# Optimization experiments

Hardware: AMD Instinct MI355X
Metric: run time of the kernel (lower is better)

Reference implementation:

```python
import jax, jax.numpy as jnp
import numpy as np

DIM = 128
HEADS = 8
DIM_HEAD = 16
INNER = DIM * DIM_HEAD  # 2048, per source: inner_dim = dim * dim_head
SCALE = DIM ** (-0.5)   # per source: scale = dim ** -0.5


def setup_inputs() -> dict:
    key = jax.random.key(0)
    k1, k2, k3, k4, k5 = jax.random.split(key, 5)
    tensor = jax.random.normal(k1, (4, 4, 1024, DIM), dtype=jnp.float32)
    latents = jax.random.normal(k2, (4, 4, 64, DIM), dtype=jnp.float32)
    # Linear(dim, inner_dim, bias=False) etc.; stored as [in, out] for x @ W
    Wq = jax.random.normal(k3, (DIM, INNER), dtype=jnp.float32) * (DIM ** -0.5)
    Wkv = jax.random.normal(k4, (DIM, 2 * INNER), dtype=jnp.float32) * (DIM ** -0.5)
    Wo = jax.random.normal(k5, (INNER, DIM), dtype=jnp.float32) * (INNER ** -0.5)
    return {"tensor": tensor, "latents": latents, "Wq": Wq, "Wkv": Wkv, "Wo": Wo}


def _split_heads(x):
    # b t n (h d) -> b h t n d
    b, t, n, hd = x.shape
    d = hd // HEADS
    return x.reshape(b, t, n, HEADS, d).transpose(0, 3, 1, 2, 4)


def reference(tensor, latents, Wq, Wkv, Wo):
    q = latents @ Wq                                  # [b,t,nl,inner]
    kv_input = jnp.concatenate((tensor, latents), axis=-2)  # [b,t,nm+nl,dim]
    kv = kv_input @ Wkv
    k, v = jnp.split(kv, 2, axis=-1)
    q, k, v = map(_split_heads, (q, k, v))            # [b,h,t,n,d]
    q = q * SCALE
    sim = jnp.einsum('bhtid,bhtjd->bhtij', q, k)
    attn = jax.nn.softmax(sim, axis=-1)               # stable softmax (matches max-subtraction)
    out = jnp.einsum('bhtij,bhtjd->bhtid', attn, v)
    # b h t n d -> b t n (h d)
    b, h, t, n, d = out.shape
    out = out.transpose(0, 2, 3, 1, 4).reshape(b, t, n, h * d)
    return out @ Wo
```

## Files before the change

### kernel.cpp

```cpp
#include <hip/hip_runtime.h>

typedef __bf16 bf16x8 __attribute__((ext_vector_type(8)));
typedef __bf16 bf16x4 __attribute__((ext_vector_type(4)));
typedef float  f32x4  __attribute__((ext_vector_type(4)));

#define SCALE2 (0.08838834764831845f * 1.4426950408889634f)

__device__ __forceinline__ f32x4 mfma16(bf16x8 a, bf16x8 b, f32x4 c) {
  return __builtin_amdgcn_mfma_f32_16x16x32_bf16(a, b, c, 0, 0, 0);
}

__device__ __forceinline__ void stage_load(const float* __restrict__ src, int tid,
                                           float4 (&r)[4]) {
  const float4* s4 = (const float4*)(src + (size_t)(tid >> 3) * 128 + ((tid & 7) << 4));
  r[0] = s4[0]; r[1] = s4[1]; r[2] = s4[2]; r[3] = s4[3];
}
__device__ __forceinline__ void stage_write(const float4 (&r)[4], __bf16 (*dst)[136],
                                            int tid) {
  const int row = tid >> 3, colb = (tid & 7) << 4;
  bf16x8 lo, hi;
  lo[0] = (__bf16)r[0].x; lo[1] = (__bf16)r[0].y; lo[2] = (__bf16)r[0].z; lo[3] = (__bf16)r[0].w;
  lo[4] = (__bf16)r[1].x; lo[5] = (__bf16)r[1].y; lo[6] = (__bf16)r[1].z; lo[7] = (__bf16)r[1].w;
  hi[0] = (__bf16)r[2].x; hi[1] = (__bf16)r[2].y; hi[2] = (__bf16)r[2].z; hi[3] = (__bf16)r[2].w;
  hi[4] = (__bf16)r[3].x; hi[5] = (__bf16)r[3].y; hi[6] = (__bf16)r[3].z; hi[7] = (__bf16)r[3].w;
  *(bf16x8*)&dst[row][colb]     = lo;
  *(bf16x8*)&dst[row][colb + 8] = hi;
}

__global__ __launch_bounds__(512, 2) void pa_attn(
    const float* __restrict__ tensor,
    const float* __restrict__ latents,
    const float* __restrict__ Wq,
    const float* __restrict__ Wkv,
    __bf16* __restrict__ Opart,
    float* __restrict__ Mpart,
    float* __restrict__ Lpart)
{
  __shared__ __align__(16) __bf16 Xs[64][136];
  __shared__ __align__(16) __bf16 Ks[64][264];
  __shared__ __align__(16) __bf16 Vts[256][72];
  __shared__ __align__(16) __bf16 Ps[8][16][40];

  const int bid = blockIdx.x;
  const int bt  = bid >> 4;
  const int h   = (bid >> 1) & 7;
  const int js  = bid & 1;

  const int tid  = threadIdx.x;
  const int wave = tid >> 6;
  const int lane = tid & 63;
  const int l15  = lane & 15;
  const int lg   = lane >> 4;
  const int it   = wave >> 1;
  const int jsub = wave & 1;

  const float* latBT = latents + (size_t)bt * (64 * 128);
  const float* tenBT = tensor  + (size_t)bt * (1024 * 128);

  {
    float4 st[4];
    stage_load(latBT, tid, st);
    stage_write(st, Xs, tid);
  }
  __syncthreads();

  #pragma unroll
  for (int n = 0; n < 2; ++n) {
    const int nt = wave * 2 + n;
    const int dcol = h * 256 + nt * 16 + l15;
    f32x4 acc[4] = {};
    #pragma unroll
    for (int kb = 0; kb < 4; ++kb) {
      const int c = kb * 32 + lg * 8;
      bf16x8 bf;
      #pragma unroll
      for (int r = 0; r < 8; ++r) bf[r] = (__bf16)Wq[(size_t)(c + r) * 2048 + dcol];
      #pragma unroll
      for (int mt = 0; mt < 4; ++mt) {
        bf16x8 af = *(const bf16x8*)&Xs[mt * 16 + l15][kb * 32 + lg * 8];
        acc[mt] = mfma16(af, bf, acc[mt]);
      }
    }
    #pragma unroll
    for (int mt = 0; mt < 4; ++mt)
      #pragma unroll
      for (int r = 0; r < 4; ++r)
        Ks[mt * 16 + lg * 4 + r][nt * 16 + l15] = (__bf16)(acc[mt][r] * SCALE2);
  }

  bf16x8 wk[2][4], wv[2][4];
  #pragma unroll
  for (int n = 0; n < 2; ++n) {
    const int dcol = h * 256 + (wave * 2 + n) * 16 + l15;
    #pragma unroll
    for (int kb = 0; kb < 4; ++kb) {
      const int c = kb * 32 + lg * 8;
      bf16x8 k8, v8;
      #pragma unroll
      for (int r = 0; r < 8; ++r) {
        k8[r] = (__bf16)Wkv[(size_t)(c + r) * 4096 + dcol];
        v8[r] = (__bf16)Wkv[(size_t)(c + r) * 4096 + 2048 + dcol];
      }
      wk[n][kb] = k8;
      wv[n][kb] = v8;
    }
  }
  __syncthreads();

  bf16x8 qf[8];
  #pragma unroll
  for (int kb = 0; kb < 8; ++kb)
    qf[kb] = *(const bf16x8*)&Ks[it * 16 + l15][kb * 32 + lg * 8];

  {
    float4 st[4];
    if (js == 0) stage_load(tenBT, tid, st);
    __syncthreads();
    if (js == 0) {
      stage_write(st, Xs, tid);
      __syncthreads();
    }
  }

  float mrow[4] = {-INFINITY, -INFINITY, -INFINITY, -INFINITY};
  float lrow[4] = {0.f, 0.f, 0.f, 0.f};
  f32x4 oacc[16] = {};

  const int NT = js ? 8 : 9;
  for (int t8 = 0; t8 < NT; ++t8) {
    const bool pf = (t8 < NT - 1);
    float4 st[4];
    if (pf) stage_load(tenBT + (size_t)((js ? 9 : 1) + t8) * (64 * 128), tid, st);

    #pragma unroll
    for (int mt = 0; mt < 4; ++mt) {
      f32x4 ka[2] = {}, va[2] = {};
      #pragma unroll
      for (int kb = 0; kb < 4; ++kb) {
        bf16x8 af = *(const bf16x8*)&Xs[mt * 16 + l15][kb * 32 + lg * 8];
        #pragma unroll
        for (int n = 0; n < 2; ++n) {
          ka[n] = mfma16(af, wk[n][kb], ka[n]);
          va[n] = mfma16(af, wv[n][kb], va[n]);
        }
      }
      #pragma unroll
      for (int n = 0; n < 2; ++n) {
        const int d = (wave * 2 + n) * 16 + l15;
        const int j = mt * 16 + lg * 4;
        #pragma unroll
        for (int r = 0; r < 4; ++r) Ks[j + r][d] = (__bf16)ka[n][r];
        bf16x4 vp;
        vp[0] = (__bf16)va[n][0]; vp[1] = (__bf16)va[n][1];
        vp[2] = (__bf16)va[n][2]; vp[3] = (__bf16)va[n][3];
        *(bf16x4*)&Vts[d][j] = vp;
      }
    }
    __syncthreads();

    f32x4 sacc[2] = {};
    #pragma unroll
    for (int kb = 0; kb < 8; ++kb) {
      #pragma unroll
      for (int jt = 0; jt < 2; ++jt) {
        bf16x8 kf = *(const bf16x8*)&Ks[jsub * 32 + jt * 16 + l15][kb * 32 + lg * 8];
        sacc[jt] = mfma16(qf[kb], kf, sacc[jt]);
      }
    }

    float alr[4];
    #pragma unroll
    for (int r = 0; r < 4; ++r) {
      float v = fmaxf(sacc[0][r], sacc[1][r]);
      v = fmaxf(v, __shfl_xor(v, 1));
      v = fmaxf(v, __shfl_xor(v, 2));
      v = fmaxf(v, __shfl_xor(v, 4));
      v = fmaxf(v, __shfl_xor(v, 8));
      const float mn = fmaxf(mrow[r], v);
      const float al = exp2f(mrow[r] - mn);
      const float p0 = exp2f(sacc[0][r] - mn);
      const float p1 = exp2f(sacc[1][r] - mn);
      sacc[0][r] = p0; sacc[1][r] = p1;
      float s = p0 + p1;
      s += __shfl_xor(s, 1);
      s += __shfl_xor(s, 2);
      s += __shfl_xor(s, 4);
      s += __shfl_xor(s, 8);
      lrow[r] = lrow[r] * al + s;
      mrow[r] = mn;
      alr[r] = al;
    }

    #pragma unroll
    for (int jt = 0; jt < 2; ++jt)
      #pragma unroll
      for (int r = 0; r < 4; ++r)
        Ps[wave][lg * 4 + r][jt * 16 + l15] = (__bf16)sacc[jt][r];

    if (pf) stage_write(st, Xs, tid);

    #pragma unroll
    for (int dt = 0; dt < 16; ++dt) {
      oacc[dt][0] *= alr[0]; oacc[dt][1] *= alr[1];
      oacc[dt][2] *= alr[2]; oacc[dt][3] *= alr[3];
    }

    asm volatile("s_waitcnt lgkmcnt(0)" ::: "memory");

    bf16x8 pfr = *(const bf16x8*)&Ps[wave][l15][lg * 8];
    #pragma unroll
    for (int dt = 0; dt < 16; ++dt) {
      bf16x8 vb = *(const bf16x8*)&Vts[dt * 16 + l15][jsub * 32 + lg * 8];
      oacc[dt] = mfma16(pfr, vb, oacc[dt]);
    }
    __syncthreads();
  }

  const int jsplit = js * 2 + jsub;
  const size_t ob = ((((size_t)jsplit * 16 + bt) * 8 + h) * 64) * 256;
  #pragma unroll
  for (int dt = 0; dt < 16; ++dt)
    #pragma unroll
    for (int r = 0; r < 4; ++r)
      Opart[ob + (size_t)(it * 16 + lg * 4 + r) * 256 + dt * 16 + l15] =
          (__bf16)oacc[dt][r];

  const size_t mb = (((size_t)jsplit * 16 + bt) * 8 + h) * 64;
  if (l15 == 0) {
    #pragma unroll
    for (int r = 0; r < 4; ++r) {
      Mpart[mb + it * 16 + lg * 4 + r] = mrow[r];
      Lpart[mb + it * 16 + lg * 4 + r] = lrow[r];
    }
  }
}

__global__ __launch_bounds__(256, 2) void pa_proj(
    const __bf16* __restrict__ Opart, const float* __restrict__ Mpart,
    const float* __restrict__ Lpart, const float* __restrict__ Wo,
    float* __restrict__ part)
{
  __shared__ float alf[4][64];
  __shared__ __align__(16) __bf16 Oh[64][264];
  __shared__ __align__(16) __bf16 Ol[64][264];

  const int bid = blockIdx.x;
  const int bt = bid >> 4, h = (bid >> 1) & 7, ch = bid & 1;
  const int tid = threadIdx.x;

  if (tid < 64) {
    const int i = tid;
    float m[4], L[4];
    #pragma unroll
    for (int s = 0; s < 4; ++s) {
      const size_t b = (((size_t)s * 16 + bt) * 8 + h) * 64 + i;
      m[s] = Mpart[b]; L[s] = Lpart[b];
    }
    const float mm = fmaxf(fmaxf(m[0], m[1]), fmaxf(m[2], m[3]));
    float a[4]; float den = 0.f;
    #pragma unroll
    for (int s = 0; s < 4; ++s) { a[s] = exp2f(m[s] - mm); den += a[s] * L[s]; }
    const float inv = 1.0f / den;
    #pragma unroll
    for (int s = 0; s < 4; ++s) alf[s][i] = a[s] * inv;
  }
  __syncthreads();

  #pragma unroll
  for (int k = 0; k < 8; ++k) {
    const int f = tid + k * 256;
    const int i = f >> 5, d8 = f & 31;
    float v[8] = {0.f, 0.f, 0.f, 0.f, 0.f, 0.f, 0.f, 0.f};
    #pragma unroll
    for (int s = 0; s < 4; ++s) {
      const float a = alf[s][i];
      bf16x8 o8 = *(const bf16x8*)&Opart[(((size_t)s * 16 + bt) * 8 + h) * 16384 +
                                         (size_t)i * 256 + d8 * 8];
      #pragma unroll
      for (int e = 0; e < 8; ++e) v[e] += a * (float)o8[e];
    }
    bf16x8 h8, l8;
    #pragma unroll
    for (int e = 0; e < 8; ++e) {
      h8[e] = (__bf16)v[e];
      l8[e] = (__bf16)(v[e] - (float)h8[e]);
    }
    *(bf16x8*)&Oh[i][d8 * 8] = h8;
    *(bf16x8*)&Ol[i][d8 * 8] = l8;
  }
  __syncthreads();

  const int wave = tid >> 6, lane = tid & 63;
  const int l15 = lane & 15, lg = lane >> 4;
  const int ncol = ch * 64 + wave * 16 + l15;
  f32x4 acc[4] = {};
  #pragma unroll
  for (int kb = 0; kb < 8; ++kb) {
    bf16x8 bh, bl;
    #pragma unroll
    for (int r = 0; r < 8; ++r) {
      const float w = Wo[(size_t)(h * 256 + kb * 32 + lg * 8 + r) * 128 + ncol];
      const __bf16 wh = (__bf16)w;
      bh[r] = wh;
      bl[r] = (__bf16)(w - (float)wh);
    }
    #pragma unroll
    for (int mt = 0; mt < 4; ++mt) {
      bf16x8 ah  = *(const bf16x8*)&Oh[mt * 16 + l15][kb * 32 + lg * 8];
      bf16x8 al8 = *(const bf16x8*)&Ol[mt * 16 + l15][kb * 32 + lg * 8];
      acc[mt] = mfma16(ah,  bh, acc[mt]);
      acc[mt] = mfma16(ah,  bl, acc[mt]);
      acc[mt] = mfma16(al8, bh, acc[mt]);
    }
  }
  const size_t pb = ((size_t)h * 16 + bt) * 8192;
  #pragma unroll
  for (int mt = 0; mt < 4; ++mt)
    #pragma unroll
    for (int r = 0; r < 4; ++r)
      part[pb + (size_t)(mt * 16 + lg * 4 + r) * 128 + ncol] = acc[mt][r];
}

__global__ __launch_bounds__(256) void pa_reduce(const float* __restrict__ part,
                                                 float* __restrict__ out) {
  const int idx = blockIdx.x * 256 + threadIdx.x;
  const f32x4* p4 = (const f32x4*)part;
  f32x4 s = p4[idx];
  #pragma unroll
  for (int h = 1; h < 8; ++h) s += p4[(size_t)h * 32768 + idx];
  ((f32x4*)out)[idx] = s;
}

extern "C" void kernel_launch(void* const* d_in, const int* in_sizes, int n_in,
                              void* d_out, int out_size, void* d_ws, size_t ws_size,
                              hipStream_t stream) {
  const float* tensor  = (const float*)d_in[0];
  const float* latents = (const float*)d_in[1];
  const float* Wq      = (const float*)d_in[2];
  const float* Wkv     = (const float*)d_in[3];
  const float* Wo      = (const float*)d_in[4];
  float* out = (float*)d_out;

  __bf16* Opart = (__bf16*)d_ws;
  float* Mpart = (float*)(Opart + (size_t)4 * 16 * 8 * 64 * 256);
  float* Lpart = Mpart + (size_t)4 * 16 * 8 * 64;
  float* part  = Lpart + (size_t)4 * 16 * 8 * 64;

  pa_attn<<<256, 512, 0, stream>>>(tensor, latents, Wq, Wkv, Opart, Mpart, Lpart);
  pa_proj<<<256, 256, 0, stream>>>(Opart, Mpart, Lpart, Wo, part);
  pa_reduce<<<128, 256, 0, stream>>>(part, out);
}
```

Baseline: 128.1 us.

## Software-pipeline K/V projection with double buffers and split output projection by inner-dim half

The attention kernel now double-buffers the X and K tiles. The next tile's K projection is computed while the current tile's scores are in flight, and its V projection after the PV step, with global loads prefetched two tiles ahead. This is meant to overlap projection MFMAs with softmax and attention work and to cut a barrier per iteration. The output-projection kernel now splits the 256-wide head dimension across the two blocks instead of splitting output columns, so each block reads only half of Opart. That doubles the number of partials the reduce kernel must sum and raises LDS use in the attention kernel.

```diff
diff --git a/kernel.cpp b/kernel.cpp
--- a/kernel.cpp
+++ b/kernel.cpp
@@ -36,8 +36,8 @@
     float* __restrict__ Mpart,
     float* __restrict__ Lpart)
 {
-  __shared__ __align__(16) __bf16 Xs[64][136];
-  __shared__ __align__(16) __bf16 Ks[64][264];
+  __shared__ __align__(16) __bf16 Xs[2][64][136];
+  __shared__ __align__(16) __bf16 Ks[2][64][264];
   __shared__ __align__(16) __bf16 Vts[256][72];
   __shared__ __align__(16) __bf16 Ps[8][16][40];
 
@@ -56,11 +56,17 @@
 
   const float* latBT = latents + (size_t)bt * (64 * 128);
   const float* tenBT = tensor  + (size_t)bt * (1024 * 128);
+  const int NT = js ? 8 : 9;
+
+  auto xsrc = [&](int tau) -> const float* {
+    return js ? (tau == 0 ? latBT : tenBT + (size_t)(8 + tau) * (64 * 128))
+              : (tenBT + (size_t)tau * (64 * 128));
+  };
 
   {
     float4 st[4];
     stage_load(latBT, tid, st);
-    stage_write(st, Xs, tid);
+    stage_write(st, Xs[0], tid);
   }
   __syncthreads();
 
@@ -77,7 +83,7 @@
       for (int r = 0; r < 8; ++r) bf[r] = (__bf16)Wq[(size_t)(c + r) * 2048 + dcol];
       #pragma unroll
       for (int mt = 0; mt < 4; ++mt) {
-        bf16x8 af = *(const bf16x8*)&Xs[mt * 16 + l15][kb * 32 + lg * 8];
+        bf16x8 af = *(const bf16x8*)&Xs[0][mt * 16 + l15][kb * 32 + lg * 8];
         acc[mt] = mfma16(af, bf, acc[mt]);
       }
     }
@@ -85,7 +91,7 @@
     for (int mt = 0; mt < 4; ++mt)
       #pragma unroll
       for (int r = 0; r < 4; ++r)
-        Ks[mt * 16 + lg * 4 + r][nt * 16 + l15] = (__bf16)(acc[mt][r] * SCALE2);
+        Ks[0][mt * 16 + lg * 4 + r][nt * 16 + l15] = (__bf16)(acc[mt][r] * SCALE2);
   }
 
   bf16x8 wk[2][4], wv[2][4];
@@ -110,61 +116,85 @@
   bf16x8 qf[8];
   #pragma unroll
   for (int kb = 0; kb < 8; ++kb)
-    qf[kb] = *(const bf16x8*)&Ks[it * 16 + l15][kb * 32 + lg * 8];
+    qf[kb] = *(const bf16x8*)&Ks[0][it * 16 + l15][kb * 32 + lg * 8];
 
   {
     float4 st[4];
-    if (js == 0) stage_load(tenBT, tid, st);
-    __syncthreads();
     if (js == 0) {
-      stage_write(st, Xs, tid);
-      __syncthreads();
-    }
-  }
+      stage_load(xsrc(0), tid, st);
+      stage_write(st, Xs[0], tid);
+    }
+    stage_load(xsrc(1), tid, st);
+    stage_write(st, Xs[1], tid);
+  }
+  __syncthreads();
+
+  #pragma unroll
+  for (int mt = 0; mt < 4; ++mt) {
+    f32x4 ka[2] = {}, va[2] = {};
+    #pragma unroll
+    for (int kb = 0; kb < 4; ++kb) {
+      bf16x8 af = *(const bf16x8*)&Xs[0][mt * 16 + l15][kb * 32 + lg * 8];
+      #pragma unroll
+      for (int n = 0; n < 2; ++n) {
+        ka[n] = mfma16(af, wk[n][kb], ka[n]);
+        va[n] = mfma16(af, wv[n][kb], va[n]);
+      }
+    }
+    #pragma unroll
+    for (int n = 0; n < 2; ++n) {
+      const int d = (wave * 2 + n) * 16 + l15;
+      const int j = mt * 16 + lg * 4;
+      #pragma unroll
+      for (int r = 0; r < 4; ++r) Ks[0][j + r][d] = (__bf16)ka[n][r];
+      bf16x4 vp;
+      vp[0] = (__bf16)va[n][0]; vp[1] = (__bf16)va[n][1];
+      vp[2] = (__bf16)va[n][2]; vp[3] = (__bf16)va[n][3];
+      *(bf16x4*)&Vts[d][j] = vp;
+    }
+  }
+  __syncthreads();
 
   float mrow[4] = {-INFINITY, -INFINITY, -INFINITY, -INFINITY};
   float lrow[4] = {0.f, 0.f, 0.f, 0.f};
   f32x4 oacc[16] = {};
 
-  const int NT = js ? 8 : 9;
-  for (int t8 = 0; t8 < NT; ++t8) {
-    const bool pf = (t8 < NT - 1);
+  for (int t = 0; t < NT; ++t) {
+    const int cb = t & 1;
+    const int nb = cb ^ 1;
+    const bool haveN  = (t + 1 < NT);
+    const bool haveN2 = (t + 2 < NT);
+
     float4 st[4];
-    if (pf) stage_load(tenBT + (size_t)((js ? 9 : 1) + t8) * (64 * 128), tid, st);
-
-    #pragma unroll
-    for (int mt = 0; mt < 4; ++mt) {
-      f32x4 ka[2] = {}, va[2] = {};
-      #pragma unroll
-      for (int kb = 0; kb < 4; ++kb) {
-        bf16x8 af = *(const bf16x8*)&Xs[mt * 16 + l15][kb * 32 + lg * 8];
+    if (haveN2) stage_load(xsrc(t + 2), tid, st);
+
+    f32x4 sacc[2] = {};
+    #pragma unroll
+    for (int kb = 0; kb < 8; ++kb) {
+      #pragma unroll
+      for (int jt = 0; jt < 2; ++jt) {
+        bf16x8 kf = *(const bf16x8*)&Ks[cb][jsub * 32 + jt * 16 + l15][kb * 32 + lg * 8];
+        sacc[jt] = mfma16(qf[kb], kf, sacc[jt]);
+      }
+    }
+
+    if (haveN) {
+      #pragma unroll
+      for (int mt = 0; mt < 4; ++mt) {
+        f32x4 ka[2] = {};
+        #pragma unroll
+        for (int kb = 0; kb < 4; ++kb) {
+          bf16x8 af = *(const bf16x8*)&Xs[nb][mt * 16 + l15][kb * 32 + lg * 8];
+          ka[0] = mfma16(af, wk[0][kb], ka[0]);
+          ka[1] = mfma16(af, wk[1][kb], ka[1]);
+        }
         #pragma unroll
         for (int n = 0; n < 2; ++n) {
-          ka[n] = mfma16(af, wk[n][kb], ka[n]);
-          va[n] = mfma16(af, wv[n][kb], va[n]);
+          const int d = (wave * 2 + n) * 16 + l15;
+          const int j = mt * 16 + lg * 4;
+          #pragma unroll
+          for (int r = 0; r < 4; ++r) Ks[nb][j + r][d] = (__bf16)ka[n][r];
         }
-      }
-      #pragma unroll
-      for (int n = 0; n < 2; ++n) {
-        const int d = (wave * 2 + n) * 16 + l15;
-        const int j = mt * 16 + lg * 4;
-        #pragma unroll
-        for (int r = 0; r < 4; ++r) Ks[j + r][d] = (__bf16)ka[n][r];
-        bf16x4 vp;
-        vp[0] = (__bf16)va[n][0]; vp[1] = (__bf16)va[n][1];
-        vp[2] = (__bf16)va[n][2]; vp[3] = (__bf16)va[n][3];
-        *(bf16x4*)&Vts[d][j] = vp;
-      }
-    }
-    __syncthreads();
-
-    f32x4 sacc[2] = {};
-    #pragma unroll
-    for (int kb = 0; kb < 8; ++kb) {
-      #pragma unroll
-      for (int jt = 0; jt < 2; ++jt) {
-        bf16x8 kf = *(const bf16x8*)&Ks[jsub * 32 + jt * 16 + l15][kb * 32 + lg * 8];
-        sacc[jt] = mfma16(qf[kb], kf, sacc[jt]);
       }
     }
 
@@ -197,7 +227,7 @@
       for (int r = 0; r < 4; ++r)
         Ps[wave][lg * 4 + r][jt * 16 + l15] = (__bf16)sacc[jt][r];
 
-    if (pf) stage_write(st, Xs, tid);
+    if (haveN2) stage_write(st, Xs[cb], tid);
 
     #pragma unroll
     for (int dt = 0; dt < 16; ++dt) {
@@ -212,6 +242,30 @@
     for (int dt = 0; dt < 16; ++dt) {
       bf16x8 vb = *(const bf16x8*)&Vts[dt * 16 + l15][jsub * 32 + lg * 8];
       oacc[dt] = mfma16(pfr, vb, oacc[dt]);
+    }
+
+    __syncthreads();
+
+    if (haveN) {
+      #pragma unroll
+      for (int mt = 0; mt < 4; ++mt) {
+        f32x4 va[2] = {};
+        #pragma unroll
+        for (int kb = 0; kb < 4; ++kb) {
+          bf16x8 af = *(const bf16x8*)&Xs[nb][mt * 16 + l15][kb * 32 + lg * 8];
+          va[0] = mfma16(af, wv[0][kb], va[0]);
+          va[1] = mfma16(af, wv[1][kb], va[1]);
+        }
+        #pragma unroll
+        for (int n = 0; n < 2; ++n) {
+          const int d = (wave * 2 + n) * 16 + l15;
+          const int j = mt * 16 + lg * 4;
+          bf16x4 vp;
+          vp[0] = (__bf16)va[n][0]; vp[1] = (__bf16)va[n][1];
+          vp[2] = (__bf16)va[n][2]; vp[3] = (__bf16)va[n][3];
+          *(bf16x4*)&Vts[d][j] = vp;
+        }
+      }
     }
     __syncthreads();
   }
@@ -241,8 +295,8 @@
     float* __restrict__ part)
 {
   __shared__ float alf[4][64];
-  __shared__ __align__(16) __bf16 Oh[64][264];
-  __shared__ __align__(16) __bf16 Ol[64][264];
+  __shared__ __align__(16) __bf16 Oh[64][136];
+  __shared__ __align__(16) __bf16 Ol[64][136];
 
   const int bid = blockIdx.x;
   const int bt = bid >> 4, h = (bid >> 1) & 7, ch = bid & 1;
@@ -267,15 +321,15 @@
   __syncthreads();
 
   #pragma unroll
-  for (int k = 0; k < 8; ++k) {
+  for (int k = 0; k < 4; ++k) {
     const int f = tid + k * 256;
-    const int i = f >> 5, d8 = f & 31;
+    const int i = f >> 4, d8 = f & 15;
     float v[8] = {0.f, 0.f, 0.f, 0.f, 0.f, 0.f, 0.f, 0.f};
     #pragma unroll
     for (int s = 0; s < 4; ++s) {
       const float a = alf[s][i];
       bf16x8 o8 = *(const bf16x8*)&Opart[(((size_t)s * 16 + bt) * 8 + h) * 16384 +
-                                         (size_t)i * 256 + d8 * 8];
+                                         (size_t)i * 256 + ch * 128 + d8 * 8];
       #pragma unroll
       for (int e = 0; e < 8; ++e) v[e] += a * (float)o8[e];
     }
@@ -292,33 +346,43 @@
 
   const int wave = tid >> 6, lane = tid & 63;
   const int l15 = lane & 15, lg = lane >> 4;
-  const int ncol = ch * 64 + wave * 16 + l15;
-  f32x4 acc[4] = {};
-  #pragma unroll
-  for (int kb = 0; kb < 8; ++kb) {
-    bf16x8 bh, bl;
-    #pragma unroll
-    for (int r = 0; r < 8; ++r) {
-      const float w = Wo[(size_t)(h * 256 + kb * 32 + lg * 8 + r) * 128 + ncol];
-      const __bf16 wh = (__bf16)w;
-      bh[r] = wh;
-      bl[r] = (__bf16)(w - (float)wh);
+  f32x4 acc[4][2] = {};
+  #pragma unroll
+  for (int kb = 0; kb < 4; ++kb) {
+    bf16x8 bh[2], bl[2];
+    #pragma unroll
+    for (int n = 0; n < 2; ++n) {
+      const int ncol = wave * 32 + n * 16 + l15;
+      #pragma unroll
+      for (int r = 0; r < 8; ++r) {
+        const float w =
+            Wo[(size_t)(h * 256 + ch * 128 + kb * 32 + lg * 8 + r) * 128 + ncol];
+        const __bf16 wh = (__bf16)w;
+        bh[n][r] = wh;
+        bl[n][r] = (__bf16)(w - (float)wh);
+      }
     }
     #pragma unroll
     for (int mt = 0; mt < 4; ++mt) {
       bf16x8 ah  = *(const bf16x8*)&Oh[mt * 16 + l15][kb * 32 + lg * 8];
       bf16x8 al8 = *(const bf16x8*)&Ol[mt * 16 + l15][kb * 32 + lg * 8];
-      acc[mt] = mfma16(ah,  bh, acc[mt]);
-      acc[mt] = mfma16(ah,  bl, acc[mt]);
-      acc[mt] = mfma16(al8, bh, acc[mt]);
-    }
-  }
-  const size_t pb = ((size_t)h * 16 + bt) * 8192;
+      #pragma unroll
+      for (int n = 0; n < 2; ++n) {
+        acc[mt][n] = mfma16(ah,  bh[n], acc[mt][n]);
+        acc[mt][n] = mfma16(ah,  bl[n], acc[mt][n]);
+        acc[mt][n] = mfma16(al8, bh[n], acc[mt][n]);
+      }
+    }
+  }
+  const size_t pb = ((size_t)(h * 2 + ch) * 16 + bt) * 8192;
   #pragma unroll
   for (int mt = 0; mt < 4; ++mt)
     #pragma unroll
-    for (int r = 0; r < 4; ++r)
-      part[pb + (size_t)(mt * 16 + lg * 4 + r) * 128 + ncol] = acc[mt][r];
+    for (int n = 0; n < 2; ++n)
+      #pragma unroll
+      for (int r = 0; r < 4; ++r)
+        part[pb + (size_t)(mt * 16 + lg * 4 + r) * 128 + wave * 32 + n * 16 + l15] =
+            acc[mt][n][r];
 }
 
 __global__ __launch_bounds__(256) void pa_reduce(const float* __restrict__ part,
@@ -327,7 +391,7 @@
   const f32x4* p4 = (const f32x4*)part;
   f32x4 s = p4[idx];
   #pragma unroll
-  for (int h = 1; h < 8; ++h) s += p4[(size_t)h * 32768 + idx];
+  for (int g = 1; g < 16; ++g) s += p4[(size_t)g * 32768 + idx];
   ((f32x4*)out)[idx] = s;
 }
 
```

Result: no change. 128.7 us (+0.5%).

## Fold K and V projections into per-head 128x128 weight products and fuse projection

Applied to the files above, without the earlier changes.

A new pre-kernel computes per-head products Wq_h·Wk_hᵀ (scaled) and Wv_h·Wo_h as 128x128 matrices stored as bf16 hi/lo pairs. The attention kernel can then score latents against the raw input tokens directly and accumulate the attention-weighted raw inputs, instead of projecting K and V to 256-dim per head for every tile. It uses MFMA against an identity to transpose input tiles, double-buffers those tiles, merges the two j-halves in shared memory and applies the output projection in place. This removes the separate partial-output kernel and its global round trip. In exchange the weight products are recomputed on every call, the grid drops to 128 blocks, each block walks all 17 tiles serially, and the split-bf16 error-compensating MFMAs add extra work.

```diff
diff --git a/kernel.cpp b/kernel.cpp
--- a/kernel.cpp
+++ b/kernel.cpp
@@ -8,6 +8,56 @@
 
 __device__ __forceinline__ f32x4 mfma16(bf16x8 a, bf16x8 b, f32x4 c) {
   return __builtin_amdgcn_mfma_f32_16x16x32_bf16(a, b, c, 0, 0, 0);
+}
+
+__global__ __launch_bounds__(256, 4) void pa_pre(
+    const float* __restrict__ Wq, const float* __restrict__ Wkv,
+    const float* __restrict__ Wo, __bf16* __restrict__ Mt,
+    __bf16* __restrict__ Nt) {
+  const int g = blockIdx.x;
+  const int mn = g >> 7, h = (g >> 4) & 7, rch = g & 15;
+  const int R = rch * 8;
+  const int tid = threadIdx.x;
+  const int hc = h * 256;
+  __shared__ float Bv[8][260];
+
+  if (mn == 0) {
+    for (int i = tid; i < 8 * 64; i += 256) {
+      const int b = i >> 6, c4 = (i & 63) * 4;
+      const float4 v = *(const float4*)&Wkv[(size_t)(R + b) * 4096 + hc + c4];
+      Bv[b][c4] = v.x; Bv[b][c4 + 1] = v.y; Bv[b][c4 + 2] = v.z; Bv[b][c4 + 3] = v.w;
+    }
+  } else {
+    for (int i = tid; i < 512; i += 256) {
+      const int c = i >> 1, q = (i & 1) * 4;
+      const float4 v = *(const float4*)&Wo[(size_t)(hc + c) * 128 + R + q];
+      Bv[q][c] = v.x; Bv[q + 1][c] = v.y; Bv[q + 2][c] = v.z; Bv[q + 3][c] = v.w;
+    }
+  }
+  __syncthreads();
+
+  const int a  = tid & 127;
+  const int bh = (tid >> 7) * 4;
+  const float* arow = (mn == 0) ? &Wq[(size_t)a * 2048 + hc]
+                                : &Wkv[(size_t)a * 4096 + 2048 + hc];
+  float acc[4] = {0.f, 0.f, 0.f, 0.f};
+  for (int c4 = 0; c4 < 256; c4 += 4) {
+    const float4 av = *(const float4*)&arow[c4];
+    #pragma unroll
+    for (int j = 0; j < 4; ++j)
+      acc[j] += av.x * Bv[bh + j][c4] + av.y * Bv[bh + j][c4 + 1] +
+                av.z * Bv[bh + j][c4 + 2] + av.w * Bv[bh + j][c4 + 3];
+  }
+  __bf16* dsth = (mn == 0 ? Mt : Nt) + (size_t)h * 16384;
+  __bf16* dstl = dsth + (size_t)8 * 16384;
+  const float sc = (mn == 0) ? SCALE2 : 1.0f;
+  #pragma unroll
+  for (int j = 0; j < 4; ++j) {
+    const float v = acc[j] * sc;
+    const __bf16 hi = (__bf16)v;
+    dsth[(size_t)(R + bh + j) * 128 + a] = hi;
+    dstl[(size_t)(R + bh + j) * 128 + a] = (__bf16)(v - (float)hi);
+  }
 }
 
 __device__ __forceinline__ void stage_load(const float* __restrict__ src, int tid,
@@ -15,7 +65,7 @@
   const float4* s4 = (const float4*)(src + (size_t)(tid >> 3) * 128 + ((tid & 7) << 4));
   r[0] = s4[0]; r[1] = s4[1]; r[2] = s4[2]; r[3] = s4[3];
 }
-__device__ __forceinline__ void stage_write(const float4 (&r)[4], __bf16 (*dst)[136],
+__device__ __forceinline__ void stage_write(const float4 (&r)[4], __bf16 (*dst)[152],
                                             int tid) {
   const int row = tid >> 3, colb = (tid & 7) << 4;
   bf16x8 lo, hi;
@@ -27,24 +77,22 @@
   *(bf16x8*)&dst[row][colb + 8] = hi;
 }
 
-__global__ __launch_bounds__(512, 2) void pa_attn(
+__global__ __launch_bounds__(512, 1) void pa_fused(
     const float* __restrict__ tensor,
     const float* __restrict__ latents,
-    const float* __restrict__ Wq,
-    const float* __restrict__ Wkv,
-    __bf16* __restrict__ Opart,
-    float* __restrict__ Mpart,
-    float* __restrict__ Lpart)
+    const __bf16* __restrict__ Mt,
+    const __bf16* __restrict__ Nt,
+    float* __restrict__ part)
 {
-  __shared__ __align__(16) __bf16 Xs[64][136];
-  __shared__ __align__(16) __bf16 Ks[64][264];
-  __shared__ __align__(16) __bf16 Vts[256][72];
+  __shared__ __align__(16) __bf16 Xs[2][64][152];
+  __shared__ __align__(16) __bf16 AsBs[2][64][136];
+  __shared__ __align__(16) __bf16 Xts[2][128][76];
   __shared__ __align__(16) __bf16 Ps[8][16][40];
-
-  const int bid = blockIdx.x;
-  const int bt  = bid >> 4;
-  const int h   = (bid >> 1) & 7;
-  const int js  = bid & 1;
+  __shared__ float Ms[8][16];
+  __shared__ float Ls[8][16];
+
+  const int bt = blockIdx.x & 15;
+  const int h  = blockIdx.x >> 4;
 
   const int tid  = threadIdx.x;
   const int wave = tid >> 6;
@@ -57,116 +105,87 @@
   const float* latBT = latents + (size_t)bt * (64 * 128);
   const float* tenBT = tensor  + (size_t)bt * (1024 * 128);
 
+  bf16x8 ident;
+  #pragma unroll
+  for (int r = 0; r < 8; ++r)
+    ident[r] = (lg * 8 + r == l15) ? (__bf16)1.0f : (__bf16)0.0f;
+
+  for (int i = tid; i < 2 * 64 * 24; i += 512) {
+    const int b = i / 1536, rem = i - b * 1536;
+    Xs[b][rem / 24][128 + rem % 24] = (__bf16)0.0f;
+  }
   {
     float4 st[4];
     stage_load(latBT, tid, st);
-    stage_write(st, Xs, tid);
-  }
-  __syncthreads();
-
-  #pragma unroll
-  for (int n = 0; n < 2; ++n) {
-    const int nt = wave * 2 + n;
-    const int dcol = h * 256 + nt * 16 + l15;
-    f32x4 acc[4] = {};
+    stage_write(st, Xs[0], tid);
+  }
+  __syncthreads();
+
+  {
+    bf16x8 mh[4], ml[4];
+    const __bf16* MtH = Mt + (size_t)h * 16384;
+    const __bf16* MtL = MtH + (size_t)8 * 16384;
     #pragma unroll
     for (int kb = 0; kb < 4; ++kb) {
-      const int c = kb * 32 + lg * 8;
-      bf16x8 bf;
-      #pragma unroll
-      for (int r = 0; r < 8; ++r) bf[r] = (__bf16)Wq[(size_t)(c + r) * 2048 + dcol];
+      mh[kb] = *(const bf16x8*)&MtH[(size_t)(wave * 16 + l15) * 128 + kb * 32 + lg * 8];
+      ml[kb] = *(const bf16x8*)&MtL[(size_t)(wave * 16 + l15) * 128 + kb * 32 + lg * 8];
+    }
+    f32x4 accA[4] = {};
+    #pragma unroll
+    for (int kb = 0; kb < 4; ++kb)
       #pragma unroll
       for (int mt = 0; mt < 4; ++mt) {
-        bf16x8 af = *(const bf16x8*)&Xs[mt * 16 + l15][kb * 32 + lg * 8];
-        acc[mt] = mfma16(af, bf, acc[mt]);
-      }
-    }
+        bf16x8 af = *(const bf16x8*)&Xs[0][mt * 16 + l15][kb * 32 + lg * 8];
+        accA[mt] = mfma16(af, mh[kb], accA[mt]);
+        accA[mt] = mfma16(af, ml[kb], accA[mt]);
+      }
     #pragma unroll
     for (int mt = 0; mt < 4; ++mt)
       #pragma unroll
-      for (int r = 0; r < 4; ++r)
-        Ks[mt * 16 + lg * 4 + r][nt * 16 + l15] = (__bf16)(acc[mt][r] * SCALE2);
-  }
-
-  bf16x8 wk[2][4], wv[2][4];
-  #pragma unroll
-  for (int n = 0; n < 2; ++n) {
-    const int dcol = h * 256 + (wave * 2 + n) * 16 + l15;
-    #pragma unroll
-    for (int kb = 0; kb < 4; ++kb) {
-      const int c = kb * 32 + lg * 8;
-      bf16x8 k8, v8;
-      #pragma unroll
-      for (int r = 0; r < 8; ++r) {
-        k8[r] = (__bf16)Wkv[(size_t)(c + r) * 4096 + dcol];
-        v8[r] = (__bf16)Wkv[(size_t)(c + r) * 4096 + 2048 + dcol];
-      }
-      wk[n][kb] = k8;
-      wv[n][kb] = v8;
-    }
-  }
-  __syncthreads();
-
-  bf16x8 qf[8];
-  #pragma unroll
-  for (int kb = 0; kb < 8; ++kb)
-    qf[kb] = *(const bf16x8*)&Ks[it * 16 + l15][kb * 32 + lg * 8];
-
-  {
-    float4 st[4];
-    if (js == 0) stage_load(tenBT, tid, st);
-    __syncthreads();
-    if (js == 0) {
-      stage_write(st, Xs, tid);
-      __syncthreads();
-    }
+      for (int r = 0; r < 4; ++r) {
+        const float v = accA[mt][r];
+        const __bf16 hi = (__bf16)v;
+        AsBs[0][mt * 16 + lg * 4 + r][wave * 16 + l15] = hi;
+        AsBs[1][mt * 16 + lg * 4 + r][wave * 16 + l15] = (__bf16)(v - (float)hi);
+      }
+  }
+  __syncthreads();
+
+  bf16x8 qh[4], ql[4];
+  #pragma unroll
+  for (int kb = 0; kb < 4; ++kb) {
+    qh[kb] = *(const bf16x8*)&AsBs[0][it * 16 + l15][kb * 32 + lg * 8];
+    ql[kb] = *(const bf16x8*)&AsBs[1][it * 16 + l15][kb * 32 + lg * 8];
   }
 
   float mrow[4] = {-INFINITY, -INFINITY, -INFINITY, -INFINITY};
   float lrow[4] = {0.f, 0.f, 0.f, 0.f};
-  f32x4 oacc[16] = {};
-
-  const int NT = js ? 8 : 9;
-  for (int t8 = 0; t8 < NT; ++t8) {
-    const bool pf = (t8 < NT - 1);
+  f32x4 oacc[8] = {};
+
+  for (int t = 0; t < 17; ++t) {
+    const int cb = t & 1, nb = cb ^ 1;
+    const bool pf = (t < 16);
     float4 st[4];
-    if (pf) stage_load(tenBT + (size_t)((js ? 9 : 1) + t8) * (64 * 128), tid, st);
-
-    #pragma unroll
-    for (int mt = 0; mt < 4; ++mt) {
-      f32x4 ka[2] = {}, va[2] = {};
-      #pragma unroll
-      for (int kb = 0; kb < 4; ++kb) {
-        bf16x8 af = *(const bf16x8*)&Xs[mt * 16 + l15][kb * 32 + lg * 8];
-        #pragma unroll
-        for (int n = 0; n < 2; ++n) {
-          ka[n] = mfma16(af, wk[n][kb], ka[n]);
-          va[n] = mfma16(af, wv[n][kb], va[n]);
-        }
-      }
-      #pragma unroll
-      for (int n = 0; n < 2; ++n) {
-        const int d = (wave * 2 + n) * 16 + l15;
-        const int j = mt * 16 + lg * 4;
-        #pragma unroll
-        for (int r = 0; r < 4; ++r) Ks[j + r][d] = (__bf16)ka[n][r];
-        bf16x4 vp;
-        vp[0] = (__bf16)va[n][0]; vp[1] = (__bf16)va[n][1];
-        vp[2] = (__bf16)va[n][2]; vp[3] = (__bf16)va[n][3];
-        *(bf16x4*)&Vts[d][j] = vp;
-      }
-    }
-    __syncthreads();
+    if (pf) stage_load(tenBT + (size_t)t * (64 * 128), tid, st);
+
+    if (t > 0) {
+      bf16x8 pfr = *(const bf16x8*)&Ps[wave][l15][lg * 8];
+      #pragma unroll
+      for (int dt = 0; dt < 8; ++dt) {
+        bf16x8 vb = *(const bf16x8*)&Xts[nb][dt * 16 + l15][jsub * 32 + lg * 8];
+        oacc[dt] = mfma16(pfr, vb, oacc[dt]);
+      }
+    }
 
     f32x4 sacc[2] = {};
     #pragma unroll
-    for (int kb = 0; kb < 8; ++kb) {
+    for (int kb = 0; kb < 4; ++kb)
       #pragma unroll
       for (int jt = 0; jt < 2; ++jt) {
-        bf16x8 kf = *(const bf16x8*)&Ks[jsub * 32 + jt * 16 + l15][kb * 32 + lg * 8];
-        sacc[jt] = mfma16(qf[kb], kf, sacc[jt]);
-      }
-    }
+        bf16x8 kf = *(const bf16x8*)&Xs[cb][jsub * 32 + jt * 16 + l15][kb * 32 + lg * 8];
+        sacc[jt] = mfma16(qh[kb], kf, sacc[jt]);
+        sacc[jt] = mfma16(ql[kb], kf, sacc[jt]);
+      }
 
     float alr[4];
     #pragma unroll
@@ -176,10 +195,10 @@
       v = fmaxf(v, __shfl_xor(v, 2));
       v = fmaxf(v, __shfl_xor(v, 4));
       v = fmaxf(v, __shfl_xor(v, 8));
-      const float mn = fmaxf(mrow[r], v);
-      const float al = exp2f(mrow[r] - mn);
-      const float p0 = exp2f(sacc[0][r] - mn);
-      const float p1 = exp2f(sacc[1][r] - mn);
+      const float mn2 = fmaxf(mrow[r], v);
+      const float al = exp2f(mrow[r] - mn2);
+      const float p0 = exp2f(sacc[0][r] - mn2);
+      const float p1 = exp2f(sacc[1][r] - mn2);
       sacc[0][r] = p0; sacc[1][r] = p1;
       float s = p0 + p1;
       s += __shfl_xor(s, 1);
@@ -187,7 +206,7 @@
       s += __shfl_xor(s, 4);
       s += __shfl_xor(s, 8);
       lrow[r] = lrow[r] * al + s;
-      mrow[r] = mn;
+      mrow[r] = mn2;
       alr[r] = al;
     }
 
@@ -197,128 +216,122 @@
       for (int r = 0; r < 4; ++r)
         Ps[wave][lg * 4 + r][jt * 16 + l15] = (__bf16)sacc[jt][r];
 
-    if (pf) stage_write(st, Xs, tid);
-
-    #pragma unroll
-    for (int dt = 0; dt < 16; ++dt) {
+    #pragma unroll
+    for (int dt = 0; dt < 8; ++dt) {
       oacc[dt][0] *= alr[0]; oacc[dt][1] *= alr[1];
       oacc[dt][2] *= alr[2]; oacc[dt][3] *= alr[3];
     }
 
-    asm volatile("s_waitcnt lgkmcnt(0)" ::: "memory");
-
+    #pragma unroll
+    for (int ds = 0; ds < 4; ++ds) {
+      const int dbase = ((wave & 1) * 4 + ds) * 16;
+      bf16x8 at = *(const bf16x8*)&Xs[cb][(wave >> 1) * 16 + l15][dbase + lg * 8];
+      f32x4 tp = mfma16(at, ident, (f32x4){0.f, 0.f, 0.f, 0.f});
+      bf16x4 tb;
+      tb[0] = (__bf16)tp[0]; tb[1] = (__bf16)tp[1];
+      tb[2] = (__bf16)tp[2]; tb[3] = (__bf16)tp[3];
+      *(bf16x4*)&Xts[cb][dbase + l15][(wave >> 1) * 16 + lg * 4] = tb;
+    }
+
+    if (pf) stage_write(st, Xs[nb], tid);
+    __syncthreads();
+  }
+
+  {
     bf16x8 pfr = *(const bf16x8*)&Ps[wave][l15][lg * 8];
     #pragma unroll
-    for (int dt = 0; dt < 16; ++dt) {
-      bf16x8 vb = *(const bf16x8*)&Vts[dt * 16 + l15][jsub * 32 + lg * 8];
+    for (int dt = 0; dt < 8; ++dt) {
+      bf16x8 vb = *(const bf16x8*)&Xts[0][dt * 16 + l15][jsub * 32 + lg * 8];
       oacc[dt] = mfma16(pfr, vb, oacc[dt]);
     }
-    __syncthreads();
-  }
-
-  const int jsplit = js * 2 + jsub;
-  const size_t ob = ((((size_t)jsplit * 16 + bt) * 8 + h) * 64) * 256;
-  #pragma unroll
-  for (int dt = 0; dt < 16; ++dt)
-    #pragma unroll
-    for (int r = 0; r < 4; ++r)
-      Opart[ob + (size_t)(it * 16 + lg * 4 + r) * 256 + dt * 16 + l15] =
-          (__bf16)oacc[dt][r];
-
-  const size_t mb = (((size_t)jsplit * 16 + bt) * 8 + h) * 64;
-  if (l15 == 0) {
+  }
+
+  if (l15 == 0)
     #pragma unroll
     for (int r = 0; r < 4; ++r) {
-      Mpart[mb + it * 16 + lg * 4 + r] = mrow[r];
-      Lpart[mb + it * 16 + lg * 4 + r] = lrow[r];
-    }
-  }
-}
-
-__global__ __launch_bounds__(256, 2) void pa_proj(
-    const __bf16* __restrict__ Opart, const float* __restrict__ Mpart,
-    const float* __restrict__ Lpart, const float* __restrict__ Wo,
-    float* __restrict__ part)
-{
-  __shared__ float alf[4][64];
-  __shared__ __align__(16) __bf16 Oh[64][264];
-  __shared__ __align__(16) __bf16 Ol[64][264];
-
-  const int bid = blockIdx.x;
-  const int bt = bid >> 4, h = (bid >> 1) & 7, ch = bid & 1;
-  const int tid = threadIdx.x;
-
-  if (tid < 64) {
-    const int i = tid;
-    float m[4], L[4];
-    #pragma unroll
-    for (int s = 0; s < 4; ++s) {
-      const size_t b = (((size_t)s * 16 + bt) * 8 + h) * 64 + i;
-      m[s] = Mpart[b]; L[s] = Lpart[b];
-    }
-    const float mm = fmaxf(fmaxf(m[0], m[1]), fmaxf(m[2], m[3]));
-    float a[4]; float den = 0.f;
-    #pragma unroll
-    for (int s = 0; s < 4; ++s) { a[s] = exp2f(m[s] - mm); den += a[s] * L[s]; }
-    const float inv = 1.0f / den;
-    #pragma unroll
-    for (int s = 0; s < 4; ++s) alf[s][i] = a[s] * inv;
-  }
-  __syncthreads();
-
-  #pragma unroll
-  for (int k = 0; k < 8; ++k) {
-    const int f = tid + k * 256;
-    const int i = f >> 5, d8 = f & 31;
-    float v[8] = {0.f, 0.f, 0.f, 0.f, 0.f, 0.f, 0.f, 0.f};
-    #pragma unroll
-    for (int s = 0; s < 4; ++s) {
-      const float a = alf[s][i];
-      bf16x8 o8 = *(const bf16x8*)&Opart[(((size_t)s * 16 + bt) * 8 + h) * 16384 +
-                                         (size_t)i * 256 + d8 * 8];
-      #pragma unroll
-      for (int e = 0; e < 8; ++e) v[e] += a * (float)o8[e];
-    }
-    bf16x8 h8, l8;
-    #pragma unroll
-    for (int e = 0; e < 8; ++e) {
-      h8[e] = (__bf16)v[e];
-      l8[e] = (__bf16)(v[e] - (float)h8[e]);
-    }
-    *(bf16x8*)&Oh[i][d8 * 8] = h8;
-    *(bf16x8*)&Ol[i][d8 * 8] = l8;
-  }
-  __syncthreads();
-
-  const int wave = tid >> 6, lane = tid & 63;
-  const int l15 = lane & 15, lg = lane >> 4;
-  const int ncol = ch * 64 + wave * 16 + l15;
-  f32x4 acc[4] = {};
-  #pragma unroll
-  for (int kb = 0; kb < 8; ++kb) {
-    bf16x8 bh, bl;
-    #pragma unroll
-    for (int r = 0; r < 8; ++r) {
-      const float w = Wo[(size_t)(h * 256 + kb * 32 + lg * 8 + r) * 128 + ncol];
-      const __bf16 wh = (__bf16)w;
-      bh[r] = wh;
-      bl[r] = (__bf16)(w - (float)wh);
-    }
-    #pragma unroll
-    for (int mt = 0; mt < 4; ++mt) {
-      bf16x8 ah  = *(const bf16x8*)&Oh[mt * 16 + l15][kb * 32 + lg * 8];
-      bf16x8 al8 = *(const bf16x8*)&Ol[mt * 16 + l15][kb * 32 + lg * 8];
-      acc[mt] = mfma16(ah,  bh, acc[mt]);
-      acc[mt] = mfma16(ah,  bl, acc[mt]);
-      acc[mt] = mfma16(al8, bh, acc[mt]);
-    }
-  }
-  const size_t pb = ((size_t)h * 16 + bt) * 8192;
-  #pragma unroll
-  for (int mt = 0; mt < 4; ++mt)
-    #pragma unroll
-    for (int r = 0; r < 4; ++r)
-      part[pb + (size_t)(mt * 16 + lg * 4 + r) * 128 + ncol] = acc[mt][r];
+      Ms[wave][lg * 4 + r] = mrow[r];
+      Ls[wave][lg * 4 + r] = lrow[r];
+    }
+  __syncthreads();
+
+  float alm[4], linv[4];
+  #pragma unroll
+  for (int r = 0; r < 4; ++r) {
+    const float mo = Ms[wave ^ 1][lg * 4 + r];
+    const float ms = fmaxf(mrow[r], mo);
+    alm[r] = exp2f(mrow[r] - ms);
+    const float alo = exp2f(mo - ms);
+    linv[r] = 1.0f / (alm[r] * lrow[r] + alo * Ls[wave ^ 1][lg * 4 + r]);
+  }
+  #pragma unroll
+  for (int dt = 0; dt < 8; ++dt) {
+    oacc[dt][0] *= alm[0]; oacc[dt][1] *= alm[1];
+    oacc[dt][2] *= alm[2]; oacc[dt][3] *= alm[3];
+  }
+  float* Os = (float*)&AsBs[0][0][0];
+  {
+    const int oh = (jsub ^ 1) * 4;
+    #pragma unroll
+    for (int dtl = 0; dtl < 4; ++dtl)
+      #pragma unroll
+      for (int r = 0; r < 4; ++r)
+        Os[(size_t)(it * 16 + lg * 4 + r) * 132 + (oh + dtl) * 16 + l15] =
+            oacc[oh + dtl][r];
+  }
+  __syncthreads();
+  float merged[4][4];
+  {
+    const int oh = jsub * 4;
+    #pragma unroll
+    for (int dtl = 0; dtl < 4; ++dtl)
+      #pragma unroll
+      for (int r = 0; r < 4; ++r)
+        merged[dtl][r] =
+            (oacc[oh + dtl][r] +
+             Os[(size_t)(it * 16 + lg * 4 + r) * 132 + (oh + dtl) * 16 + l15]) *
+            linv[r];
+  }
+  __syncthreads();
+  #pragma unroll
+  for (int dtl = 0; dtl < 4; ++dtl)
+    #pragma unroll
+    for (int r = 0; r < 4; ++r) {
+      const float v = merged[dtl][r];
+      const __bf16 hi = (__bf16)v;
+      AsBs[0][it * 16 + lg * 4 + r][jsub * 64 + dtl * 16 + l15] = hi;
+      AsBs[1][it * 16 + lg * 4 + r][jsub * 64 + dtl * 16 + l15] =
+          (__bf16)(v - (float)hi);
+    }
+  __syncthreads();
+
+  {
+    bf16x8 nh[4], nl[4];
+    const __bf16* NtH = Nt + (size_t)h * 16384;
+    const __bf16* NtL = NtH + (size_t)8 * 16384;
+    #pragma unroll
+    for (int kb = 0; kb < 4; ++kb) {
+      nh[kb] = *(const bf16x8*)&NtH[(size_t)(wave * 16 + l15) * 128 + kb * 32 + lg * 8];
+      nl[kb] = *(const bf16x8*)&NtL[(size_t)(wave * 16 + l15) * 128 + kb * 32 + lg * 8];
+    }
+    f32x4 pacc[4] = {};
+    #pragma unroll
+    for (int kb = 0; kb < 4; ++kb)
+      #pragma unroll
+      for (int mt = 0; mt < 4; ++mt) {
+        bf16x8 ah = *(const bf16x8*)&AsBs[0][mt * 16 + l15][kb * 32 + lg * 8];
+        bf16x8 al = *(const bf16x8*)&AsBs[1][mt * 16 + l15][kb * 32 + lg * 8];
+        pacc[mt] = mfma16(ah, nh[kb], pacc[mt]);
+        pacc[mt] = mfma16(al, nh[kb], pacc[mt]);
+        pacc[mt] = mfma16(ah, nl[kb], pacc[mt]);
+      }
+    const size_t pb = ((size_t)h * 16 + bt) * 8192;
+    #pragma unroll
+    for (int mt = 0; mt < 4; ++mt)
+      #pragma unroll
+      for (int r = 0; r < 4; ++r)
+        part[pb + (size_t)(mt * 16 + lg * 4 + r) * 128 + wave * 16 + l15] =
+            pacc[mt][r];
+  }
 }
 
 __global__ __launch_bounds__(256) void pa_reduce(const float* __restrict__ part,
@@ -327,7 +340,7 @@
   const f32x4* p4 = (const f32x4*)part;
   f32x4 s = p4[idx];
   #pragma unroll
-  for (int h = 1; h < 8; ++h) s += p4[(size_t)h * 32768 + idx];
+  for (int g = 1; g < 8; ++g) s += p4[(size_t)g * 32768 + idx];
   ((f32x4*)out)[idx] = s;
 }
 
@@ -341,12 +354,11 @@
   const float* Wo      = (const float*)d_in[4];
   float* out = (float*)d_out;
 
-  __bf16* Opart = (__bf16*)d_ws;
-  float* Mpart = (float*)(Opart + (size_t)4 * 16 * 8 * 64 * 256);
-  float* Lpart = Mpart + (size_t)4 * 16 * 8 * 64;
-  float* part  = Lpart + (size_t)4 * 16 * 8 * 64;
-
-  pa_attn<<<256, 512, 0, stream>>>(tensor, latents, Wq, Wkv, Opart, Mpart, Lpart);
-  pa_proj<<<256, 256, 0, stream>>>(Opart, Mpart, Lpart, Wo, part);
+  __bf16* Mt  = (__bf16*)d_ws;
+  __bf16* Nt  = Mt + (size_t)2 * 8 * 128 * 128;
+  float*  part = (float*)(Nt + (size_t)2 * 8 * 128 * 128);
+
+  pa_pre<<<256, 256, 0, stream>>>(Wq, Wkv, Wo, Mt, Nt);
+  pa_fused<<<128, 512, 0, stream>>>(tensor, latents, Mt, Nt, part);
   pa_reduce<<<128, 256, 0, stream>>>(part, out);
 }
```

Measured after the change: 125.9 us. No clear change (-1.7%).
